# Performance work log

Hardware: AMD Instinct MI355X
Metric: run time of the kernel (lower is better)

The kernel has to match this reference:

```python
import jax, jax.numpy as jnp
import numpy as np

N = 40000          # nodes
E = 640000         # directed edges (before self-loops)
NEG_SLOPE = 0.2    # PyG GATConv default negative_slope


def _segment_softmax(e, dst, n):
    # e: [E, H] per-edge logits, softmax over edges sharing the same dst
    m = jax.ops.segment_max(e, dst, num_segments=n)          # [n, H]
    ex = jnp.exp(e - m[dst])
    s = jax.ops.segment_sum(ex, dst, num_segments=n)         # [n, H]
    return ex / (s[dst] + 1e-16)


def _gat_layer(x, src, dst, W, att_src, att_dst, bias, heads, out_ch, concat, n):
    h = (x @ W).reshape(n, heads, out_ch)                    # [n, H, C]
    a_s = jnp.einsum('nhc,hc->nh', h, att_src)               # [n, H]
    a_d = jnp.einsum('nhc,hc->nh', h, att_dst)
    e = jax.nn.leaky_relu(a_s[src] + a_d[dst], NEG_SLOPE)    # [E, H]
    alpha = _segment_softmax(e, dst, n)                      # [E, H]
    msg = h[src] * alpha[:, :, None]                         # [E, H, C]
    out = jax.ops.segment_sum(msg, dst, num_segments=n)      # [n, H, C]
    out = out.reshape(n, heads * out_ch) if concat else out.mean(axis=1)
    return out + bias


def setup_inputs():
    key = jax.random.key(0)
    ks = jax.random.split(key, 12)
    x = jax.random.normal(ks[0], (N, 128), dtype=jnp.float32)
    edge_index = jax.random.randint(ks[1], (2, E), 0, N, dtype=jnp.int64)
    weights = jax.random.uniform(ks[2], (E,), dtype=jnp.float32)
    # GATConv(128, 64, heads=2)
    W1 = jax.random.normal(ks[3], (128, 2 * 64), dtype=jnp.float32) * 0.1
    att_src1 = jax.random.normal(ks[4], (2, 64), dtype=jnp.float32) * 0.1
    att_dst1 = jax.random.normal(ks[5], (2, 64), dtype=jnp.float32) * 0.1
    b1 = jnp.zeros((128,), dtype=jnp.float32)
    # GATConv(128, 4, heads=1, concat=False)
    W2 = jax.random.normal(ks[6], (128, 4), dtype=jnp.float32) * 0.1
    att_src2 = jax.random.normal(ks[7], (1, 4), dtype=jnp.float32) * 0.1
    att_dst2 = jax.random.normal(ks[8], (1, 4), dtype=jnp.float32) * 0.1
    b2 = jnp.zeros((4,), dtype=jnp.float32)
    return {'x': x, 'edge_index': edge_index, 'weights': weights,
            'W1': W1, 'att_src1': att_src1, 'att_dst1': att_dst1, 'b1': b1,
            'W2': W2, 'att_src2': att_src2, 'att_dst2': att_dst2, 'b2': b2}


def reference(x, edge_index, weights, W1, att_src1, att_dst1, b1, W2, att_src2, att_dst2, b2):
    # PyG default add_self_loops=True
    loop = jnp.arange(N, dtype=edge_index.dtype)
    src = jnp.concatenate([edge_index[0], loop])
    dst = jnp.concatenate([edge_index[1], loop])
    # dropout layers are identity in eval mode; `weights` unused (as in source)
    h = _gat_layer(x, src, dst, W1, att_src1, att_dst1, b1, 2, 64, True, N)
    h = jax.nn.elu(h)
    h = _gat_layer(h, src, dst, W2, att_src2, att_dst2, b2, 1, 4, False, N)
    return jax.nn.softmax(h, axis=1)
```

## Files before the change

### kernel.cpp

```cpp
#include <hip/hip_runtime.h>
#include <hip/hip_bf16.h>
#include <math.h>

#define N_NODES 40000
#define N_EDGES 640000
#define ET (N_EDGES + N_NODES)
#define CAP 64

__device__ __forceinline__ float wave_red_sum(float v) {
#pragma unroll
  for (int m = 32; m >= 1; m >>= 1) v += __shfl_xor(v, m, 64);
  return v;
}
__device__ __forceinline__ float half_red_sum(float v) {
#pragma unroll
  for (int m = 16; m >= 1; m >>= 1) v += __shfl_xor(v, m, 64);
  return v;
}
__device__ __forceinline__ float red16(float v) {
#pragma unroll
  for (int m = 8; m >= 1; m >>= 1) v += __shfl_xor(v, m, 64);
  return v;
}

__global__ void k_build(const int* __restrict__ ei, int* __restrict__ deg,
                        int* __restrict__ csr_src) {
  int i = blockIdx.x * blockDim.x + threadIdx.x;
  if (i >= ET) return;
  int s, d;
  if (i < N_EDGES) { s = ei[i]; d = ei[N_EDGES + i]; }
  else             { s = d = i - N_EDGES; }
  int r = atomicAdd(&deg[d], 1);
  if (r < CAP) csr_src[(d << 6) + r] = s;
}

__global__ __launch_bounds__(256) void k_gemm1(
    const float* __restrict__ x, const float* __restrict__ W1,
    const float* __restrict__ asv, const float* __restrict__ adv,
    __hip_bfloat16* __restrict__ h1b, float* __restrict__ a_s, float* __restrict__ a_d) {
  __shared__ float xs[32 * 128];
  int t = threadIdx.x;
  int n0 = blockIdx.x * 32;
  {
    const float4* xg = (const float4*)(x + (size_t)n0 * 128);
    float4* xs4 = (float4*)xs;
#pragma unroll
    for (int i = 0; i < 4; i++) xs4[t + i * 256] = xg[t + i * 256];
  }
  __syncthreads();

  int lane = t & 63;
  int g = t >> 6;
  int c0 = lane * 2;
  const float4* xs4 = (const float4*)(xs + (size_t)g * 8 * 128);

  float2 acc[8];
#pragma unroll
  for (int j = 0; j < 8; j++) acc[j] = make_float2(0.f, 0.f);

  float2 w0 = *(const float2*)(W1 + (size_t)0 * 128 + c0);
  float2 w1 = *(const float2*)(W1 + (size_t)1 * 128 + c0);
  float2 w2 = *(const float2*)(W1 + (size_t)2 * 128 + c0);
  float2 w3 = *(const float2*)(W1 + (size_t)3 * 128 + c0);

  for (int k4 = 0; k4 < 32; k4++) {
    float2 nw0, nw1, nw2, nw3;
    if (k4 < 31) {
      nw0 = *(const float2*)(W1 + (size_t)(4 * k4 + 4) * 128 + c0);
      nw1 = *(const float2*)(W1 + (size_t)(4 * k4 + 5) * 128 + c0);
      nw2 = *(const float2*)(W1 + (size_t)(4 * k4 + 6) * 128 + c0);
      nw3 = *(const float2*)(W1 + (size_t)(4 * k4 + 7) * 128 + c0);
    }
#pragma unroll
    for (int j = 0; j < 8; j++) {
      float4 xv = xs4[j * 32 + k4];
      acc[j].x = fmaf(xv.x, w0.x, acc[j].x);
      acc[j].y = fmaf(xv.x, w0.y, acc[j].y);
      acc[j].x = fmaf(xv.y, w1.x, acc[j].x);
      acc[j].y = fmaf(xv.y, w1.y, acc[j].y);
      acc[j].x = fmaf(xv.z, w2.x, acc[j].x);
      acc[j].y = fmaf(xv.z, w2.y, acc[j].y);
      acc[j].x = fmaf(xv.w, w3.x, acc[j].x);
      acc[j].y = fmaf(xv.w, w3.y, acc[j].y);
    }
    w0 = nw0; w1 = nw1; w2 = nw2; w3 = nw3;
  }

  float2 av_s = *(const float2*)(asv + c0);
  float2 av_d = *(const float2*)(adv + c0);
  int head = lane >> 5;
#pragma unroll
  for (int j = 0; j < 8; j++) {
    int n = n0 + g * 8 + j;
    __hip_bfloat162 hv;
    hv.x = __float2bfloat16(acc[j].x);
    hv.y = __float2bfloat16(acc[j].y);
    *(__hip_bfloat162*)(h1b + (size_t)n * 128 + c0) = hv;
    float rs = half_red_sum(acc[j].x * av_s.x + acc[j].y * av_s.y);
    float rd = half_red_sum(acc[j].x * av_d.x + acc[j].y * av_d.y);
    if ((lane & 31) == 0) {
      a_s[n * 2 + head] = rs;
      a_d[n * 2 + head] = rd;
    }
  }
}

__global__ __launch_bounds__(256) void k_agg1(
    const int* __restrict__ deg, const int* __restrict__ csr_src,
    const float* __restrict__ a_s, const float* __restrict__ a_d,
    const __hip_bfloat16* __restrict__ h1b, const float* __restrict__ b1,
    const float* __restrict__ W2, const float* __restrict__ as2,
    const float* __restrict__ ad2,
    float* __restrict__ h2pack, float* __restrict__ a_d2) {
  int wv = threadIdx.x >> 6;
  int v = blockIdx.x * 4 + wv;
  int lane = threadIdx.x & 63;
  int head = lane >> 5;
  int dg = min(deg[v], CAP);
  float2 Ad = *(const float2*)(a_d + 2 * v);
  const __hip_bfloat162* h1b2 = (const __hip_bfloat162*)h1b;

  __shared__ int    lds_s[4][64];
  __shared__ float2 lds_e[4][64];

  int sreg = 0;
  float ex0 = 0.f, ex1 = 0.f;
  if (lane < dg) {
    sreg = csr_src[(v << 6) + lane];
    float2 As = *(const float2*)(a_s + 2 * sreg);
    float e0 = As.x + Ad.x; e0 = (e0 >= 0.f) ? e0 : 0.2f * e0;
    float e1 = As.y + Ad.y; e1 = (e1 >= 0.f) ? e1 : 0.2f * e1;
    ex0 = __expf(e0); ex1 = __expf(e1);
  }
  float sum0 = wave_red_sum(ex0);
  float sum1 = wave_red_sum(ex1);
  lds_s[wv][lane] = sreg;
  lds_e[wv][lane] = make_float2(ex0, ex1);
  __threadfence_block();

  float acc0 = 0.f, acc1 = 0.f;
  int j = 0;
  for (; j + 8 <= dg; j += 8) {
    int s0 = lds_s[wv][j + 0], s1 = lds_s[wv][j + 1];
    int s2 = lds_s[wv][j + 2], s3 = lds_s[wv][j + 3];
    int s4 = lds_s[wv][j + 4], s5 = lds_s[wv][j + 5];
    int s6 = lds_s[wv][j + 6], s7 = lds_s[wv][j + 7];
    __hip_bfloat162 h0 = h1b2[(size_t)s0 * 64 + lane];
    __hip_bfloat162 h1 = h1b2[(size_t)s1 * 64 + lane];
    __hip_bfloat162 h2 = h1b2[(size_t)s2 * 64 + lane];
    __hip_bfloat162 h3 = h1b2[(size_t)s3 * 64 + lane];
    __hip_bfloat162 h4 = h1b2[(size_t)s4 * 64 + lane];
    __hip_bfloat162 h5 = h1b2[(size_t)s5 * 64 + lane];
    __hip_bfloat162 h6 = h1b2[(size_t)s6 * 64 + lane];
    __hip_bfloat162 h7 = h1b2[(size_t)s7 * 64 + lane];
#pragma unroll
    for (int q = 0; q < 8; q++) {
      float2 wq = lds_e[wv][j + q];
      float eq = head ? wq.y : wq.x;
      __hip_bfloat162 hq = (q == 0) ? h0 : (q == 1) ? h1 : (q == 2) ? h2 :
                           (q == 3) ? h3 : (q == 4) ? h4 : (q == 5) ? h5 :
                           (q == 6) ? h6 : h7;
      acc0 = fmaf(eq, __bfloat162float(hq.x), acc0);
      acc1 = fmaf(eq, __bfloat162float(hq.y), acc1);
    }
  }
  for (; j + 4 <= dg; j += 4) {
    int s0 = lds_s[wv][j + 0], s1 = lds_s[wv][j + 1];
    int s2 = lds_s[wv][j + 2], s3 = lds_s[wv][j + 3];
    __hip_bfloat162 h0 = h1b2[(size_t)s0 * 64 + lane];
    __hip_bfloat162 h1 = h1b2[(size_t)s1 * 64 + lane];
    __hip_bfloat162 h2 = h1b2[(size_t)s2 * 64 + lane];
    __hip_bfloat162 h3 = h1b2[(size_t)s3 * 64 + lane];
    float2 w0 = lds_e[wv][j + 0], w1 = lds_e[wv][j + 1];
    float2 w2 = lds_e[wv][j + 2], w3 = lds_e[wv][j + 3];
    float e0 = head ? w0.y : w0.x, e1 = head ? w1.y : w1.x;
    float e2 = head ? w2.y : w2.x, e3 = head ? w3.y : w3.x;
    acc0 = fmaf(e0, __bfloat162float(h0.x), acc0);
    acc1 = fmaf(e0, __bfloat162float(h0.y), acc1);
    acc0 = fmaf(e1, __bfloat162float(h1.x), acc0);
    acc1 = fmaf(e1, __bfloat162float(h1.y), acc1);
    acc0 = fmaf(e2, __bfloat162float(h2.x), acc0);
    acc1 = fmaf(e2, __bfloat162float(h2.y), acc1);
    acc0 = fmaf(e3, __bfloat162float(h3.x), acc0);
    acc1 = fmaf(e3, __bfloat162float(h3.y), acc1);
  }
  for (; j < dg; j++) {
    int s = lds_s[wv][j];
    float2 wq = lds_e[wv][j];
    float ex = head ? wq.y : wq.x;
    __hip_bfloat162 hv = h1b2[(size_t)s * 64 + lane];
    acc0 = fmaf(ex, __bfloat162float(hv.x), acc0);
    acc1 = fmaf(ex, __bfloat162float(hv.y), acc1);
  }

  float inv = 1.f / ((head ? sum1 : sum0) + 1e-16f);
  float2 bv = *(const float2*)(b1 + 2 * lane);
  float o0 = acc0 * inv + bv.x;
  float o1 = acc1 * inv + bv.y;
  o0 = (o0 > 0.f) ? o0 : expm1f(o0);
  o1 = (o1 > 0.f) ? o1 : expm1f(o1);

  float4 wA = *(const float4*)(W2 + (2 * lane) * 4);
  float4 wB = *(const float4*)(W2 + (2 * lane + 1) * 4);
  float p0 = wave_red_sum(o0 * wA.x + o1 * wB.x);
  float p1 = wave_red_sum(o0 * wA.y + o1 * wB.y);
  float p2 = wave_red_sum(o0 * wA.z + o1 * wB.z);
  float p3 = wave_red_sum(o0 * wA.w + o1 * wB.w);
  if (lane == 0) {
    float4 q = {p0, p1, p2, p3};
    *(float4*)(h2pack + (size_t)v * 8) = q;
    h2pack[(size_t)v * 8 + 4] =
        p0 * as2[0] + p1 * as2[1] + p2 * as2[2] + p3 * as2[3];
    a_d2[v] = p0 * ad2[0] + p1 * ad2[1] + p2 * ad2[2] + p3 * ad2[3];
  }
}

__global__ __launch_bounds__(256) void k_agg2(
    const int* __restrict__ deg, const int* __restrict__ csr_src,
    const float* __restrict__ h2pack, const float* __restrict__ a_d,
    const float* __restrict__ b2, float* __restrict__ out) {
  int t = threadIdx.x;
  int grp = t >> 4, gl = t & 15;
  int v = blockIdx.x * 16 + grp;
  int dg = min(deg[v], CAP);
  float adv = a_d[v];
  const float4* pk = (const float4*)h2pack;

  float sum = 0.f;
  float4 acc = {0.f, 0.f, 0.f, 0.f};
  for (int i = gl; i < dg; i += 16) {
    int s = csr_src[(v << 6) + i];
    float4 r0 = pk[2 * s];
    float4 r1 = pk[2 * s + 1];
    float e = r1.x + adv;
    e = (e >= 0.f) ? e : 0.2f * e;
    float ex = __expf(e);
    sum += ex;
    acc.x = fmaf(ex, r0.x, acc.x);
    acc.y = fmaf(ex, r0.y, acc.y);
    acc.z = fmaf(ex, r0.z, acc.z);
    acc.w = fmaf(ex, r0.w, acc.w);
  }
  sum = red16(sum);
  acc.x = red16(acc.x);
  acc.y = red16(acc.y);
  acc.z = red16(acc.z);
  acc.w = red16(acc.w);

  if (gl == 0) {
    float invd = 1.f / (sum + 1e-16f);
    float o0 = acc.x * invd + b2[0];
    float o1 = acc.y * invd + b2[1];
    float o2 = acc.z * invd + b2[2];
    float o3 = acc.w * invd + b2[3];
    float mx = fmaxf(fmaxf(o0, o1), fmaxf(o2, o3));
    float e0 = __expf(o0 - mx), e1 = __expf(o1 - mx);
    float e2 = __expf(o2 - mx), e3 = __expf(o3 - mx);
    float s4 = e0 + e1 + e2 + e3;
    float4 r = {e0 / s4, e1 / s4, e2 / s4, e3 / s4};
    *(float4*)(out + (size_t)v * 4) = r;
  }
}

extern "C" void kernel_launch(void* const* d_in, const int* in_sizes, int n_in,
                              void* d_out, int out_size, void* d_ws, size_t ws_size,
                              hipStream_t stream) {
  const float* x   = (const float*)d_in[0];
  const int*   ei  = (const int*)d_in[1];
  const float* W1  = (const float*)d_in[3];
  const float* as1 = (const float*)d_in[4];
  const float* ad1 = (const float*)d_in[5];
  const float* b1  = (const float*)d_in[6];
  const float* W2  = (const float*)d_in[7];
  const float* as2 = (const float*)d_in[8];
  const float* ad2 = (const float*)d_in[9];
  const float* b2  = (const float*)d_in[10];
  float* out = (float*)d_out;

  char* w = (char*)d_ws;
  auto alloc = [&](size_t bytes) {
    char* p = w;
    w += (bytes + 255) & ~(size_t)255;
    return p;
  };
  int*   deg     = (int*)alloc((size_t)N_NODES * 4);
  int*   csr_src = (int*)alloc((size_t)N_NODES * CAP * 4);
  __hip_bfloat16* h1b = (__hip_bfloat16*)alloc((size_t)N_NODES * 128 * 2);
  float* a_s1w   = (float*)alloc((size_t)N_NODES * 2 * 4);
  float* a_d1w   = (float*)alloc((size_t)N_NODES * 2 * 4);
  float* h2pack  = (float*)alloc((size_t)N_NODES * 8 * 4);
  float* a_d2w   = (float*)alloc((size_t)N_NODES * 4);

  hipMemsetAsync(deg, 0, (size_t)N_NODES * 4, stream);
  k_build<<<(ET + 255) / 256, 256, 0, stream>>>(ei, deg, csr_src);
  k_gemm1<<<N_NODES / 32, 256, 0, stream>>>(x, W1, as1, ad1, h1b, a_s1w, a_d1w);
  k_agg1<<<N_NODES / 4, 256, 0, stream>>>(deg, csr_src, a_s1w, a_d1w, h1b, b1,
                                          W2, as2, ad2, h2pack, a_d2w);
  k_agg2<<<N_NODES / 16, 256, 0, stream>>>(deg, csr_src, h2pack, a_d2w, b2, out);
}
```

Measured before the change: 200.7 us.

## Fuse all stages into one cooperative persistent kernel with grid syncs

Replaces the memset and four separate kernel launches with a single cooperative persistent kernel that zeroes degrees, runs CSR build and GEMM concurrently on split halves of the grid, then aggregates both layers, separated by grid-wide syncs. The aim is to remove launch gaps and tail effects between small kernels and to overlap the atomic-bound build with the compute-bound GEMM. It also unrolls the 8-edge inner loop explicitly. In exchange it adds grid.sync costs, an occupancy query on the host for each call, and persistent grid-stride loops that may balance load less well. The original multi-kernel path is kept as a fallback.

```diff
diff --git a/kernel.cpp b/kernel.cpp
--- a/kernel.cpp
+++ b/kernel.cpp
@@ -1,11 +1,15 @@
 #include <hip/hip_runtime.h>
 #include <hip/hip_bf16.h>
+#include <hip/hip_cooperative_groups.h>
 #include <math.h>
+
+namespace cg = cooperative_groups;
 
 #define N_NODES 40000
 #define N_EDGES 640000
 #define ET (N_EDGES + N_NODES)
 #define CAP 64
+#define NTHR 256
 
 __device__ __forceinline__ float wave_red_sum(float v) {
 #pragma unroll
@@ -23,37 +27,25 @@
   return v;
 }
 
-__global__ void k_build(const int* __restrict__ ei, int* __restrict__ deg,
-                        int* __restrict__ csr_src) {
-  int i = blockIdx.x * blockDim.x + threadIdx.x;
-  if (i >= ET) return;
-  int s, d;
-  if (i < N_EDGES) { s = ei[i]; d = ei[N_EDGES + i]; }
-  else             { s = d = i - N_EDGES; }
-  int r = atomicAdd(&deg[d], 1);
-  if (r < CAP) csr_src[(d << 6) + r] = s;
-}
-
-__global__ __launch_bounds__(256) void k_gemm1(
+
+__device__ __forceinline__ void gemm_tile(
+    int tile, int t, int lane, int wv, float* xs,
     const float* __restrict__ x, const float* __restrict__ W1,
     const float* __restrict__ asv, const float* __restrict__ adv,
-    __hip_bfloat16* __restrict__ h1b, float* __restrict__ a_s, float* __restrict__ a_d) {
-  __shared__ float xs[32 * 128];
-  int t = threadIdx.x;
-  int n0 = blockIdx.x * 32;
+    __hip_bfloat16* __restrict__ h1b, float* __restrict__ a_s,
+    float* __restrict__ a_d) {
+  int n0 = tile * 32;
+  int c0 = lane * 2;
+  __syncthreads();
   {
     const float4* xg = (const float4*)(x + (size_t)n0 * 128);
-    float4* xs4 = (float4*)xs;
-#pragma unroll
-    for (int i = 0; i < 4; i++) xs4[t + i * 256] = xg[t + i * 256];
+    float4* xs4w = (float4*)xs;
+#pragma unroll
+    for (int i = 0; i < 4; i++) xs4w[t + i * 256] = xg[t + i * 256];
   }
   __syncthreads();
 
-  int lane = t & 63;
-  int g = t >> 6;
-  int c0 = lane * 2;
-  const float4* xs4 = (const float4*)(xs + (size_t)g * 8 * 128);
-
+  const float4* xs4 = (const float4*)(xs + (size_t)wv * 8 * 128);
   float2 acc[8];
 #pragma unroll
   for (int j = 0; j < 8; j++) acc[j] = make_float2(0.f, 0.f);
@@ -91,7 +83,7 @@
   int head = lane >> 5;
 #pragma unroll
   for (int j = 0; j < 8; j++) {
-    int n = n0 + g * 8 + j;
+    int n = n0 + wv * 8 + j;
     __hip_bfloat162 hv;
     hv.x = __float2bfloat16(acc[j].x);
     hv.y = __float2bfloat16(acc[j].y);
@@ -105,23 +97,18 @@
   }
 }
 
-__global__ __launch_bounds__(256) void k_agg1(
+__device__ __forceinline__ void agg1_node(
+    int v, int lane, int wv, int* lds_s_w, float2* lds_e_w,
     const int* __restrict__ deg, const int* __restrict__ csr_src,
     const float* __restrict__ a_s, const float* __restrict__ a_d,
     const __hip_bfloat16* __restrict__ h1b, const float* __restrict__ b1,
     const float* __restrict__ W2, const float* __restrict__ as2,
     const float* __restrict__ ad2,
     float* __restrict__ h2pack, float* __restrict__ a_d2) {
-  int wv = threadIdx.x >> 6;
-  int v = blockIdx.x * 4 + wv;
-  int lane = threadIdx.x & 63;
   int head = lane >> 5;
   int dg = min(deg[v], CAP);
   float2 Ad = *(const float2*)(a_d + 2 * v);
   const __hip_bfloat162* h1b2 = (const __hip_bfloat162*)h1b;
-
-  __shared__ int    lds_s[4][64];
-  __shared__ float2 lds_e[4][64];
 
   int sreg = 0;
   float ex0 = 0.f, ex1 = 0.f;
@@ -134,17 +121,17 @@
   }
   float sum0 = wave_red_sum(ex0);
   float sum1 = wave_red_sum(ex1);
-  lds_s[wv][lane] = sreg;
-  lds_e[wv][lane] = make_float2(ex0, ex1);
+  lds_s_w[lane] = sreg;
+  lds_e_w[lane] = make_float2(ex0, ex1);
   __threadfence_block();
 
   float acc0 = 0.f, acc1 = 0.f;
   int j = 0;
   for (; j + 8 <= dg; j += 8) {
-    int s0 = lds_s[wv][j + 0], s1 = lds_s[wv][j + 1];
-    int s2 = lds_s[wv][j + 2], s3 = lds_s[wv][j + 3];
-    int s4 = lds_s[wv][j + 4], s5 = lds_s[wv][j + 5];
-    int s6 = lds_s[wv][j + 6], s7 = lds_s[wv][j + 7];
+    int s0 = lds_s_w[j + 0], s1 = lds_s_w[j + 1];
+    int s2 = lds_s_w[j + 2], s3 = lds_s_w[j + 3];
+    int s4 = lds_s_w[j + 4], s5 = lds_s_w[j + 5];
+    int s6 = lds_s_w[j + 6], s7 = lds_s_w[j + 7];
     __hip_bfloat162 h0 = h1b2[(size_t)s0 * 64 + lane];
     __hip_bfloat162 h1 = h1b2[(size_t)s1 * 64 + lane];
     __hip_bfloat162 h2 = h1b2[(size_t)s2 * 64 + lane];
@@ -153,26 +140,40 @@
     __hip_bfloat162 h5 = h1b2[(size_t)s5 * 64 + lane];
     __hip_bfloat162 h6 = h1b2[(size_t)s6 * 64 + lane];
     __hip_bfloat162 h7 = h1b2[(size_t)s7 * 64 + lane];
-#pragma unroll
-    for (int q = 0; q < 8; q++) {
-      float2 wq = lds_e[wv][j + q];
-      float eq = head ? wq.y : wq.x;
-      __hip_bfloat162 hq = (q == 0) ? h0 : (q == 1) ? h1 : (q == 2) ? h2 :
-                           (q == 3) ? h3 : (q == 4) ? h4 : (q == 5) ? h5 :
-                           (q == 6) ? h6 : h7;
-      acc0 = fmaf(eq, __bfloat162float(hq.x), acc0);
-      acc1 = fmaf(eq, __bfloat162float(hq.y), acc1);
-    }
+    float2 w0 = lds_e_w[j + 0], w1 = lds_e_w[j + 1];
+    float2 w2 = lds_e_w[j + 2], w3 = lds_e_w[j + 3];
+    float2 w4 = lds_e_w[j + 4], w5 = lds_e_w[j + 5];
+    float2 w6 = lds_e_w[j + 6], w7 = lds_e_w[j + 7];
+    float e0 = head ? w0.y : w0.x, e1 = head ? w1.y : w1.x;
+    float e2 = head ? w2.y : w2.x, e3 = head ? w3.y : w3.x;
+    float e4 = head ? w4.y : w4.x, e5 = head ? w5.y : w5.x;
+    float e6 = head ? w6.y : w6.x, e7 = head ? w7.y : w7.x;
+    acc0 = fmaf(e0, __bfloat162float(h0.x), acc0);
+    acc1 = fmaf(e0, __bfloat162float(h0.y), acc1);
+    acc0 = fmaf(e1, __bfloat162float(h1.x), acc0);
+    acc1 = fmaf(e1, __bfloat162float(h1.y), acc1);
+    acc0 = fmaf(e2, __bfloat162float(h2.x), acc0);
+    acc1 = fmaf(e2, __bfloat162float(h2.y), acc1);
+    acc0 = fmaf(e3, __bfloat162float(h3.x), acc0);
+    acc1 = fmaf(e3, __bfloat162float(h3.y), acc1);
+    acc0 = fmaf(e4, __bfloat162float(h4.x), acc0);
+    acc1 = fmaf(e4, __bfloat162float(h4.y), acc1);
+    acc0 = fmaf(e5, __bfloat162float(h5.x), acc0);
+    acc1 = fmaf(e5, __bfloat162float(h5.y), acc1);
+    acc0 = fmaf(e6, __bfloat162float(h6.x), acc0);
+    acc1 = fmaf(e6, __bfloat162float(h6.y), acc1);
+    acc0 = fmaf(e7, __bfloat162float(h7.x), acc0);
+    acc1 = fmaf(e7, __bfloat162float(h7.y), acc1);
   }
   for (; j + 4 <= dg; j += 4) {
-    int s0 = lds_s[wv][j + 0], s1 = lds_s[wv][j + 1];
-    int s2 = lds_s[wv][j + 2], s3 = lds_s[wv][j + 3];
+    int s0 = lds_s_w[j + 0], s1 = lds_s_w[j + 1];
+    int s2 = lds_s_w[j + 2], s3 = lds_s_w[j + 3];
     __hip_bfloat162 h0 = h1b2[(size_t)s0 * 64 + lane];
     __hip_bfloat162 h1 = h1b2[(size_t)s1 * 64 + lane];
     __hip_bfloat162 h2 = h1b2[(size_t)s2 * 64 + lane];
     __hip_bfloat162 h3 = h1b2[(size_t)s3 * 64 + lane];
-    float2 w0 = lds_e[wv][j + 0], w1 = lds_e[wv][j + 1];
-    float2 w2 = lds_e[wv][j + 2], w3 = lds_e[wv][j + 3];
+    float2 w0 = lds_e_w[j + 0], w1 = lds_e_w[j + 1];
+    float2 w2 = lds_e_w[j + 2], w3 = lds_e_w[j + 3];
     float e0 = head ? w0.y : w0.x, e1 = head ? w1.y : w1.x;
     float e2 = head ? w2.y : w2.x, e3 = head ? w3.y : w3.x;
     acc0 = fmaf(e0, __bfloat162float(h0.x), acc0);
@@ -185,8 +186,8 @@
     acc1 = fmaf(e3, __bfloat162float(h3.y), acc1);
   }
   for (; j < dg; j++) {
-    int s = lds_s[wv][j];
-    float2 wq = lds_e[wv][j];
+    int s = lds_s_w[j];
+    float2 wq = lds_e_w[j];
     float ex = head ? wq.y : wq.x;
     __hip_bfloat162 hv = h1b2[(size_t)s * 64 + lane];
     acc0 = fmaf(ex, __bfloat162float(hv.x), acc0);
@@ -215,15 +216,12 @@
   }
 }
 
-__global__ __launch_bounds__(256) void k_agg2(
-    const int* __restrict__ deg, const int* __restrict__ csr_src,
-    const float* __restrict__ h2pack, const float* __restrict__ a_d,
+__device__ __forceinline__ void agg2_node(
+    int v, int gl, const int* __restrict__ deg, const int* __restrict__ csr_src,
+    const float* __restrict__ h2pack, const float* __restrict__ a_d2,
     const float* __restrict__ b2, float* __restrict__ out) {
-  int t = threadIdx.x;
-  int grp = t >> 4, gl = t & 15;
-  int v = blockIdx.x * 16 + grp;
   int dg = min(deg[v], CAP);
-  float adv = a_d[v];
+  float adv2 = a_d2[v];
   const float4* pk = (const float4*)h2pack;
 
   float sum = 0.f;
@@ -232,7 +230,7 @@
     int s = csr_src[(v << 6) + i];
     float4 r0 = pk[2 * s];
     float4 r1 = pk[2 * s + 1];
-    float e = r1.x + adv;
+    float e = r1.x + adv2;
     e = (e >= 0.f) ? e : 0.2f * e;
     float ex = __expf(e);
     sum += ex;
@@ -260,6 +258,111 @@
     float4 r = {e0 / s4, e1 / s4, e2 / s4, e3 / s4};
     *(float4*)(out + (size_t)v * 4) = r;
   }
+}
+
+__global__ __launch_bounds__(NTHR, 4) void k_mega(
+    const float* __restrict__ x, const int* __restrict__ ei,
+    const float* __restrict__ W1, const float* __restrict__ asv,
+    const float* __restrict__ adv, const float* __restrict__ b1,
+    const float* __restrict__ W2, const float* __restrict__ as2,
+    const float* __restrict__ ad2, const float* __restrict__ b2,
+    int* __restrict__ deg, int* __restrict__ csr_src,
+    __hip_bfloat16* __restrict__ h1b, float* __restrict__ a_s,
+    float* __restrict__ a_d, float* __restrict__ h2pack,
+    float* __restrict__ a_d2, float* __restrict__ out) {
+  cg::grid_group grid = cg::this_grid();
+  int t = threadIdx.x;
+  int bid = blockIdx.x;
+  int gdim = gridDim.x;
+  int lane = t & 63;
+  int wv = t >> 6;
+
+  __shared__ float xs[32 * 128];
+  __shared__ int    lds_s[4][64];
+  __shared__ float2 lds_e[4][64];
+
+  for (int i = bid * NTHR + t; i < N_NODES; i += gdim * NTHR) deg[i] = 0;
+  __threadfence();
+  grid.sync();
+
+  int half = gdim >> 1;
+  bool firstH = (bid < half);
+  int hb = firstH ? bid : bid - half;
+
+  auto do_build = [&](int lo, int hi) {
+    for (int i = lo + hb * NTHR + t; i < hi; i += half * NTHR) {
+      int s, d;
+      if (i < N_EDGES) { s = ei[i]; d = ei[N_EDGES + i]; }
+      else             { s = d = i - N_EDGES; }
+      int r = atomicAdd(&deg[d], 1);
+      if (r < CAP) csr_src[(d << 6) + r] = s;
+    }
+  };
+  auto do_gemm = [&](int tlo, int thi) {
+    for (int tile = tlo + hb; tile < thi; tile += half)
+      gemm_tile(tile, t, lane, wv, xs, x, W1, asv, adv, h1b, a_s, a_d);
+  };
+
+  if (firstH) { do_build(0, ET / 2); do_gemm(625, 1250); }
+  else        { do_gemm(0, 625);     do_build(ET / 2, ET); }
+
+  __threadfence();
+  grid.sync();
+
+  for (int gq = bid; gq < N_NODES / 4; gq += gdim)
+    agg1_node(gq * 4 + wv, lane, wv, lds_s[wv], lds_e[wv],
+              deg, csr_src, a_s, a_d, h1b, b1, W2, as2, ad2, h2pack, a_d2);
+
+  __threadfence();
+  grid.sync();
+
+  {
+    int grp = t >> 4, gl = t & 15;
+    for (int gq = bid; gq < N_NODES / 16; gq += gdim)
+      agg2_node(gq * 16 + grp, gl, deg, csr_src, h2pack, a_d2, b2, out);
+  }
+}
+
+__global__ void k_build(const int* __restrict__ ei, int* __restrict__ deg,
+                        int* __restrict__ csr_src) {
+  int i = blockIdx.x * blockDim.x + threadIdx.x;
+  if (i >= ET) return;
+  int s, d;
+  if (i < N_EDGES) { s = ei[i]; d = ei[N_EDGES + i]; }
+  else             { s = d = i - N_EDGES; }
+  int r = atomicAdd(&deg[d], 1);
+  if (r < CAP) csr_src[(d << 6) + r] = s;
+}
+
+__global__ __launch_bounds__(256) void k_gemm1(
+    const float* __restrict__ x, const float* __restrict__ W1,
+    const float* __restrict__ asv, const float* __restrict__ adv,
+    __hip_bfloat16* __restrict__ h1b, float* __restrict__ a_s, float* __restrict__ a_d) {
+  __shared__ float xs[32 * 128];
+  int t = threadIdx.x;
+  gemm_tile(blockIdx.x, t, t & 63, t >> 6, xs, x, W1, asv, adv, h1b, a_s, a_d);
+}
+
+__global__ __launch_bounds__(256) void k_agg1(
+    const int* __restrict__ deg, const int* __restrict__ csr_src,
+    const float* __restrict__ a_s, const float* __restrict__ a_d,
+    const __hip_bfloat16* __restrict__ h1b, const float* __restrict__ b1,
+    const float* __restrict__ W2, const float* __restrict__ as2,
+    const float* __restrict__ ad2,
+    float* __restrict__ h2pack, float* __restrict__ a_d2) {
+  __shared__ int    lds_s[4][64];
+  __shared__ float2 lds_e[4][64];
+  int wv = threadIdx.x >> 6;
+  agg1_node(blockIdx.x * 4 + wv, threadIdx.x & 63, wv, lds_s[wv], lds_e[wv],
+            deg, csr_src, a_s, a_d, h1b, b1, W2, as2, ad2, h2pack, a_d2);
+}
+
+__global__ __launch_bounds__(256) void k_agg2(
+    const int* __restrict__ deg, const int* __restrict__ csr_src,
+    const float* __restrict__ h2pack, const float* __restrict__ a_d2,
+    const float* __restrict__ b2, float* __restrict__ out) {
+  int t = threadIdx.x;
+  agg2_node(blockIdx.x * 16 + (t >> 4), t & 15, deg, csr_src, h2pack, a_d2, b2, out);
 }
 
 extern "C" void kernel_launch(void* const* d_in, const int* in_sizes, int n_in,
@@ -291,10 +394,34 @@
   float* h2pack  = (float*)alloc((size_t)N_NODES * 8 * 4);
   float* a_d2w   = (float*)alloc((size_t)N_NODES * 4);
 
-  hipMemsetAsync(deg, 0, (size_t)N_NODES * 4, stream);
-  k_build<<<(ET + 255) / 256, 256, 0, stream>>>(ei, deg, csr_src);
-  k_gemm1<<<N_NODES / 32, 256, 0, stream>>>(x, W1, as1, ad1, h1b, a_s1w, a_d1w);
-  k_agg1<<<N_NODES / 4, 256, 0, stream>>>(deg, csr_src, a_s1w, a_d1w, h1b, b1,
-                                          W2, as2, ad2, h2pack, a_d2w);
-  k_agg2<<<N_NODES / 16, 256, 0, stream>>>(deg, csr_src, h2pack, a_d2w, b2, out);
-}
+  int blocksPerCU = 0;
+  hipError_t qerr = hipOccupancyMaxActiveBlocksPerMultiprocessor(
+      &blocksPerCU, (const void*)k_mega, NTHR, 0);
+  int grid = 0;
+  if (qerr == hipSuccess && blocksPerCU > 0) {
+    grid = blocksPerCU * 256;
+    if (grid > 1024) grid = 1024;
+    grid &= ~1;
+  }
+
+  hipError_t lerr = hipErrorUnknown;
+  if (grid >= 2) {
+    void* kargs[] = {
+      (void*)&x, (void*)&ei, (void*)&W1, (void*)&as1, (void*)&ad1, (void*)&b1,
+      (void*)&W2, (void*)&as2, (void*)&ad2, (void*)&b2,
+      (void*)&deg, (void*)&csr_src, (void*)&h1b, (void*)&a_s1w, (void*)&a_d1w,
+      (void*)&h2pack, (void*)&a_d2w, (void*)&out
+    };
+    lerr = hipLaunchCooperativeKernel((void*)k_mega, dim3(grid), dim3(NTHR),
+                                      kargs, 0, stream);
+  }
+
+  if (lerr != hipSuccess) {
+    hipMemsetAsync(deg, 0, (size_t)N_NODES * 4, stream);
+    k_build<<<(ET + 255) / 256, 256, 0, stream>>>(ei, deg, csr_src);
+    k_gemm1<<<N_NODES / 32, 256, 0, stream>>>(x, W1, as1, ad1, h1b, a_s1w, a_d1w);
+    k_agg1<<<N_NODES / 4, 256, 0, stream>>>(deg, csr_src, a_s1w, a_d1w, h1b, b1,
+                                            W2, as2, ad2, h2pack, a_d2w);
+    k_agg2<<<N_NODES / 16, 256, 0, stream>>>(deg, csr_src, h2pack, a_d2w, b2, out);
+  }
+}
```

New measurement: 517.1 us. 2.58x slower.
